# Kernel optimization log

Hardware: AMD Instinct MI355X
Metric: run time of the kernel (lower is better)

## Reference

```python
import jax, jax.numpy as jnp
import numpy as np

HEADS = 4
DIM_HEAD = 64
SCALE = DIM_HEAD ** -0.5


def setup_inputs() -> dict:
    key = jax.random.key(0)
    k1, k2, k3 = jax.random.split(key, 3)
    C = 256
    hidden = HEADS * DIM_HEAD  # 256
    x = jax.random.normal(k1, (16, C, 64, 64), dtype=jnp.float32)
    # 1x1 conv weights collapsed to [out, in] matrices
    w_qkv = jax.random.normal(k2, (3 * hidden, C), dtype=jnp.float32) * (C ** -0.5)
    w_out = jax.random.normal(k3, (C, hidden), dtype=jnp.float32) * (hidden ** -0.5)
    b_out = jnp.zeros((C,), dtype=jnp.float32)
    return {"x": x, "w_qkv": w_qkv, "w_out": w_out, "b_out": b_out}


def reference(x, w_qkv, w_out, b_out):
    b, c, h, w = x.shape
    n = h * w
    # 1x1 conv == channel GEMM
    qkv = jnp.einsum('bchw,oc->bohw', x, w_qkv)           # [b, 3*hidden, h, w]
    qkv = qkv.reshape(b, 3, HEADS, DIM_HEAD, n)            # [b, 3, H, d, n]
    q, k, v = qkv[:, 0], qkv[:, 1], qkv[:, 2]              # each [b, H, d, n]
    q = jax.nn.softmax(q, axis=2) * SCALE                  # softmax over d
    k = jax.nn.softmax(k, axis=3)                          # softmax over n
    context = jnp.einsum('bhdn,bhen->bhde', k, v)          # [b, H, d, e]
    out = jnp.einsum('bhde,bhdn->bhen', context, q)        # [b, H, e, n]
    out = out.reshape(b, HEADS * DIM_HEAD, h, w)           # [b, hidden, h, w]
    return jnp.einsum('bchw,oc->bohw', out, w_out) + b_out[None, :, None, None]
```

## Files before the change

### kernel.cpp

```cpp
#include <hip/hip_runtime.h>

#define NPIX 4096
#define SCALE 0.125f

typedef _Float16 half8 __attribute__((ext_vector_type(8)));
typedef _Float16 half4 __attribute__((ext_vector_type(4)));
typedef float floatx4 __attribute__((ext_vector_type(4)));

__device__ __forceinline__ void async16(void* lds, const void* g) {
  __builtin_amdgcn_global_load_lds(
      (const __attribute__((address_space(1))) unsigned int*)(uintptr_t)g,
      (__attribute__((address_space(3))) unsigned int*)(unsigned)(uintptr_t)lds,
      16, 0, 0);
}

__global__ __launch_bounds__(256) void split16_kernel(const float* __restrict__ w,
                                                      _Float16* __restrict__ hi,
                                                      _Float16* __restrict__ lo, int n) {
  int i = blockIdx.x * 256 + threadIdx.x;
  if (i < n) {
    float v = w[i];
    _Float16 h = (_Float16)v;
    hi[i] = h;
    lo[i] = (_Float16)(v - (float)h);
  }
}

__global__ __launch_bounds__(256) void transpose16_kernel(const float* __restrict__ x,
                                                          _Float16* __restrict__ xt) {
  __shared__ float t[64][65];
  const int n0 = blockIdx.x * 64, c0 = blockIdx.y * 64, b = blockIdx.z;
  const float* xp = x + (long)b * 256 * NPIX;
  const int tid = threadIdx.x;
  const int r = tid >> 4, c4 = (tid & 15) * 4;
#pragma unroll
  for (int p = 0; p < 4; p++) {
    float4 v = *(const float4*)&xp[(long)(c0 + r + p * 16) * NPIX + n0 + c4];
    t[r + p * 16][c4 + 0] = v.x;
    t[r + p * 16][c4 + 1] = v.y;
    t[r + p * 16][c4 + 2] = v.z;
    t[r + p * 16][c4 + 3] = v.w;
  }
  __syncthreads();
  const int n = tid >> 2, cg = (tid & 3) * 16;
  alignas(16) _Float16 o[16];
#pragma unroll
  for (int i = 0; i < 16; i++) o[i] = (_Float16)t[cg + i][n];
  _Float16* dst = &xt[((long)b * NPIX + n0 + n) * 256 + c0 + cg];
  *(float4*)dst = *(float4*)&o[0];
  *(float4*)(dst + 8) = *(float4*)&o[8];
}

__global__ __launch_bounds__(256) void q_gemm_softmax(const _Float16* __restrict__ Ahp,
                                                      const _Float16* __restrict__ Alp,
                                                      const _Float16* __restrict__ Bt,
                                                      _Float16* __restrict__ PT) {
  union alignas(16) QU {
    struct {
      _Float16 Ah[128 * 32];
      _Float16 Al[128 * 32];
      _Float16 Bt[128 * 32];
    } st;
    _Float16 pt[128][128];
  };
  __shared__ QU u;
  const int tid = threadIdx.x;
  const int n0 = blockIdx.x * 128, m0 = blockIdx.y * 128;
  const int bz = blockIdx.z;
  const _Float16* Bp = Bt + (long)bz * NPIX * 256;
  const int wv = tid >> 6, l = tid & 63;
  const int r16 = l & 15, q = l >> 4;
  const int mb = (wv >> 1) * 64, nb = (wv & 1) * 64;
  const int r1 = tid >> 2;
  const int o1 = ((tid & 3) * 8) ^ (((r1 >> 1) & 3) * 8);
  const int r2 = r1 + 64;
  const int ldsc1 = (wv * 64) * 8;
  const int ldsc2 = (256 + wv * 64) * 8;
  const int q8 = (q * 8) ^ (((r16 >> 1) & 3) * 8);

  floatx4 acc[4][4];
#pragma unroll
  for (int i = 0; i < 4; i++)
#pragma unroll
    for (int j = 0; j < 4; j++) acc[i][j] = (floatx4){0.f, 0.f, 0.f, 0.f};

  for (int kt = 0; kt < 8; kt++) {
    const int k0 = kt * 32;
    async16(&u.st.Ah[ldsc1], &Ahp[(long)(m0 + r1) * 256 + k0 + o1]);
    async16(&u.st.Ah[ldsc2], &Ahp[(long)(m0 + r2) * 256 + k0 + o1]);
    async16(&u.st.Al[ldsc1], &Alp[(long)(m0 + r1) * 256 + k0 + o1]);
    async16(&u.st.Al[ldsc2], &Alp[(long)(m0 + r2) * 256 + k0 + o1]);
    async16(&u.st.Bt[ldsc1], &Bp[(long)(n0 + r1) * 256 + k0 + o1]);
    async16(&u.st.Bt[ldsc2], &Bp[(long)(n0 + r2) * 256 + k0 + o1]);
    __syncthreads();
    half8 fa[4], flo[4], fb[4];
#pragma unroll
    for (int i = 0; i < 4; i++) {
      fa[i] = *(const half8*)&u.st.Ah[(mb + i * 16 + r16) * 32 + q8];
      flo[i] = *(const half8*)&u.st.Al[(mb + i * 16 + r16) * 32 + q8];
      fb[i] = *(const half8*)&u.st.Bt[(nb + i * 16 + r16) * 32 + q8];
    }
#pragma unroll
    for (int i = 0; i < 4; i++)
#pragma unroll
      for (int j = 0; j < 4; j++) {
        acc[i][j] = __builtin_amdgcn_mfma_f32_16x16x32_f16(fa[i], fb[j], acc[i][j], 0, 0, 0);
        acc[i][j] = __builtin_amdgcn_mfma_f32_16x16x32_f16(flo[i], fb[j], acc[i][j], 0, 0, 0);
      }
    __syncthreads();
  }

#pragma unroll
  for (int j = 0; j < 4; j++) {
    float s = 0.f;
#pragma unroll
    for (int i = 0; i < 4; i++)
#pragma unroll
      for (int t = 0; t < 4; t++) {
        float e = __expf(acc[i][j][t]);
        acc[i][j][t] = e;
        s += e;
      }
    s += __shfl_xor(s, 16, 64);
    s += __shfl_xor(s, 32, 64);
    const float rinv = 1.0f / s;
    const int nl = nb + j * 16 + r16;
    const int swz = (nl & 7) * 8;
#pragma unroll
    for (int i = 0; i < 4; i++) {
      half4 h4;
#pragma unroll
      for (int t = 0; t < 4; t++) h4[t] = (_Float16)(acc[i][j][t] * rinv);
      *(half4*)&u.pt[nl][(mb + i * 16 + q * 4) ^ swz] = h4;
    }
  }
  __syncthreads();
  const int rbase = tid >> 4, c16 = tid & 15;
  _Float16* dst = PT + ((long)(bz * 2 + (m0 >> 7)) * NPIX + n0) * 128;
#pragma unroll
  for (int k = 0; k < 8; k++) {
    const int row = rbase + k * 16;
    const int chunk = c16 ^ (row & 7);
    float4 v = *(const float4*)&u.pt[row][chunk * 8];
    *(float4*)&dst[(long)row * 128 + c16 * 8] = v;
  }
}

__global__ __launch_bounds__(256) void kv_ctx_gemm(const _Float16* __restrict__ Ahp,
                                                   const _Float16* __restrict__ Alp,
                                                   const _Float16* __restrict__ Bt,
                                                   float* __restrict__ pbuf,
                                                   float* __restrict__ rsbuf) {
  union alignas(16) KVU {
    struct {
      _Float16 Ah[128 * 32];
      _Float16 Al[128 * 32];
      _Float16 Bt[128 * 32];
    } st;
    _Float16 ev[128][136];
  };
  __shared__ KVU u;
  const int tid = threadIdx.x;
  const int chunk = blockIdx.x;
  const int hi = blockIdx.y;
  const int b = blockIdx.z;
  const int n0 = chunk * 128;
  const _Float16* Bp = Bt + (long)b * NPIX * 256;
  const int wv = tid >> 6, l = tid & 63;
  const int r16 = l & 15, q = l >> 4;
  const int mb = (wv >> 1) * 64, nb = (wv & 1) * 64;
  const int r1 = tid >> 2;
  const int o1 = ((tid & 3) * 8) ^ (((r1 >> 1) & 3) * 8);
  const int ldsc1 = (wv * 64) * 8;
  const int ldsc2 = (256 + wv * 64) * 8;
  const int q8 = (q * 8) ^ (((r16 >> 1) & 3) * 8);
  const long gAk = (long)(256 + hi * 64 + r1) * 256;
  const long gAv = (long)(512 + hi * 64 + r1) * 256;

  floatx4 acc[4][4];
#pragma unroll
  for (int i = 0; i < 4; i++)
#pragma unroll
    for (int j = 0; j < 4; j++) acc[i][j] = (floatx4){0.f, 0.f, 0.f, 0.f};

  for (int kt = 0; kt < 8; kt++) {
    const int k0 = kt * 32;
    async16(&u.st.Ah[ldsc1], &Ahp[gAk + k0 + o1]);
    async16(&u.st.Ah[ldsc2], &Ahp[gAv + k0 + o1]);
    async16(&u.st.Al[ldsc1], &Alp[gAk + k0 + o1]);
    async16(&u.st.Al[ldsc2], &Alp[gAv + k0 + o1]);
    async16(&u.st.Bt[ldsc1], &Bp[(long)(n0 + r1) * 256 + k0 + o1]);
    async16(&u.st.Bt[ldsc2], &Bp[(long)(n0 + 64 + r1) * 256 + k0 + o1]);
    __syncthreads();
    half8 fa[4], flo[4], fb[4];
#pragma unroll
    for (int i = 0; i < 4; i++) {
      fa[i] = *(const half8*)&u.st.Ah[(mb + i * 16 + r16) * 32 + q8];
      flo[i] = *(const half8*)&u.st.Al[(mb + i * 16 + r16) * 32 + q8];
      fb[i] = *(const half8*)&u.st.Bt[(nb + i * 16 + r16) * 32 + q8];
    }
#pragma unroll
    for (int i = 0; i < 4; i++)
#pragma unroll
      for (int j = 0; j < 4; j++) {
        acc[i][j] = __builtin_amdgcn_mfma_f32_16x16x32_f16(fa[i], fb[j], acc[i][j], 0, 0, 0);
        acc[i][j] = __builtin_amdgcn_mfma_f32_16x16x32_f16(flo[i], fb[j], acc[i][j], 0, 0, 0);
      }
    __syncthreads();
  }

  const bool is_k = (mb == 0);
#pragma unroll
  for (int i = 0; i < 4; i++) {
    const int row = mb + i * 16 + q * 4;
#pragma unroll
    for (int j = 0; j < 4; j++) {
      const int col = nb + j * 16 + r16;
#pragma unroll
      for (int t = 0; t < 4; t++) {
        const float vv0 = acc[i][j][t];
        u.ev[row + t][col] = (_Float16)(is_k ? __expf(vv0) : vv0);
      }
    }
  }
  __syncthreads();

  floatx4 c2[4];
#pragma unroll
  for (int j = 0; j < 4; j++) c2[j] = (floatx4){0.f, 0.f, 0.f, 0.f};
  float rs = 0.f;
#pragma unroll
  for (int ks = 0; ks < 4; ks++) {
    half8 a = *(const half8*)&u.ev[wv * 16 + r16][ks * 32 + q * 8];
#pragma unroll
    for (int ii = 0; ii < 8; ii++) rs += (float)a[ii];
#pragma unroll
    for (int j = 0; j < 4; j++) {
      half8 bv = *(const half8*)&u.ev[64 + j * 16 + r16][ks * 32 + q * 8];
      c2[j] = __builtin_amdgcn_mfma_f32_16x16x32_f16(a, bv, c2[j], 0, 0, 0);
    }
  }
  rs += __shfl_xor(rs, 16, 64);
  rs += __shfl_xor(rs, 32, 64);
  const int bh = b * 4 + hi;
  float* pp = pbuf + ((long)bh * 32 + chunk) * 4096;
#pragma unroll
  for (int j = 0; j < 4; j++)
#pragma unroll
    for (int reg = 0; reg < 4; reg++)
      pp[(wv * 16 + q * 4 + reg) * 64 + j * 16 + r16] = c2[j][reg];
  if (l < 16) rsbuf[((long)bh * 32 + chunk) * 64 + wv * 16 + r16] = rs;
}

__global__ __launch_bounds__(256) void reduce_ctx(const float* __restrict__ pbuf,
                                                  float* __restrict__ ctx) {
  int g = blockIdx.x * 256 + threadIdx.x;
  int bh = g >> 12, e = g & 4095;
  const float* pp = pbuf + ((long)bh * 32) * 4096 + e;
  float s = 0.f;
#pragma unroll
  for (int c = 0; c < 32; c++) s += pp[(long)c * 4096];
  ctx[g] = s;
}

__global__ __launch_bounds__(256) void zinv_kernel(const float* __restrict__ rsbuf,
                                                   float* __restrict__ kinvz) {
  int g = blockIdx.x * 256 + threadIdx.x;
  int bh = g >> 6, d = g & 63;
  const float* rp = rsbuf + (long)bh * 32 * 64 + d;
  float s = 0.f;
#pragma unroll
  for (int c = 0; c < 32; c++) s += rp[c * 64];
  kinvz[g] = 1.0f / s;
}

__global__ __launch_bounds__(256) void mctx_kernel(const float* __restrict__ w_out,
                                                   const float* __restrict__ ctx,
                                                   const float* __restrict__ kinvz,
                                                   _Float16* __restrict__ Mhi,
                                                   _Float16* __restrict__ Mlo) {
  __shared__ float sctxT[64][65];
  const int cq = blockIdx.x, h = blockIdx.y, b = blockIdx.z;
  const int bh = b * 4 + h;
  const float* cp = ctx + (long)bh * 4096;
  const int tid = threadIdx.x;
  {
    const int d = tid >> 2, e0 = (tid & 3) * 16;
#pragma unroll
    for (int k = 0; k < 4; k++) {
      float4 v = *(const float4*)&cp[d * 64 + e0 + k * 4];
      sctxT[e0 + k * 4 + 0][d] = v.x;
      sctxT[e0 + k * 4 + 1][d] = v.y;
      sctxT[e0 + k * 4 + 2][d] = v.z;
      sctxT[e0 + k * 4 + 3][d] = v.w;
    }
  }
  __syncthreads();
  const int c = cq * 64 + (tid >> 2);
  const int d0 = (tid & 3) * 16;
  const float* wp = w_out + (long)c * 256 + h * 64;
  float acc[16];
#pragma unroll
  for (int i = 0; i < 16; i++) acc[i] = 0.f;
#pragma unroll
  for (int e4 = 0; e4 < 16; e4++) {
    float4 wv = *(const float4*)&wp[e4 * 4];
#pragma unroll
    for (int u2 = 0; u2 < 4; u2++) {
      const float we = ((const float*)&wv)[u2];
      const int e = e4 * 4 + u2;
#pragma unroll
      for (int dd = 0; dd < 16; dd++) acc[dd] = fmaf(we, sctxT[e][d0 + dd], acc[dd]);
    }
  }
  alignas(16) _Float16 hi16[16], lo16[16];
#pragma unroll
  for (int k4 = 0; k4 < 4; k4++) {
    float4 zv = *(const float4*)&kinvz[bh * 64 + d0 + k4 * 4];
#pragma unroll
    for (int u2 = 0; u2 < 4; u2++) {
      const int dd = k4 * 4 + u2;
      float v = acc[dd] * (SCALE * ((const float*)&zv)[u2]);
      _Float16 hh = (_Float16)v;
      hi16[dd] = hh;
      lo16[dd] = (_Float16)(v - (float)hh);
    }
  }
  _Float16* mh = Mhi + ((long)b * 256 + c) * 256 + h * 64 + d0;
  _Float16* ml = Mlo + ((long)b * 256 + c) * 256 + h * 64 + d0;
#pragma unroll
  for (int k = 0; k < 2; k++) {
    *(float4*)&mh[k * 8] = *(float4*)&hi16[k * 8];
    *(float4*)&ml[k * 8] = *(float4*)&lo16[k * 8];
  }
}

__global__ __launch_bounds__(256) void out_gemm(const _Float16* __restrict__ Mhi,
                                                const _Float16* __restrict__ Mlo,
                                                const _Float16* __restrict__ PT,
                                                float* __restrict__ C,
                                                const float* __restrict__ bias) {
  __shared__ _Float16 sAh[128 * 32];
  __shared__ _Float16 sAl[128 * 32];
  __shared__ _Float16 sBt[128 * 32];
  const int tid = threadIdx.x;
  const int n0 = blockIdx.x * 128, m0 = blockIdx.y * 128;
  const int b = blockIdx.z;
  const _Float16* Ah = Mhi + (long)b * 65536;
  const _Float16* Al = Mlo + (long)b * 65536;
  float* Cp = C + (long)b * 256 * NPIX;
  const int wv = tid >> 6, l = tid & 63;
  const int r16 = l & 15, q = l >> 4;
  const int mb = (wv >> 1) * 64, nb = (wv & 1) * 64;
  const int r1 = tid >> 2;
  const int o1 = ((tid & 3) * 8) ^ (((r1 >> 1) & 3) * 8);
  const int r2 = r1 + 64;
  const int ldsc1 = (wv * 64) * 8;
  const int ldsc2 = (256 + wv * 64) * 8;
  const int q8 = (q * 8) ^ (((r16 >> 1) & 3) * 8);

  floatx4 acc[4][4];
#pragma unroll
  for (int i = 0; i < 4; i++)
#pragma unroll
    for (int j = 0; j < 4; j++) acc[i][j] = (floatx4){0.f, 0.f, 0.f, 0.f};

  for (int kt = 0; kt < 8; kt++) {
    const int k0 = kt * 32;
    async16(&sAh[ldsc1], &Ah[(long)(m0 + r1) * 256 + k0 + o1]);
    async16(&sAh[ldsc2], &Ah[(long)(m0 + r2) * 256 + k0 + o1]);
    async16(&sAl[ldsc1], &Al[(long)(m0 + r1) * 256 + k0 + o1]);
    async16(&sAl[ldsc2], &Al[(long)(m0 + r2) * 256 + k0 + o1]);
    const _Float16* Bk = PT + ((long)(b * 2 + (kt >> 2)) * NPIX + n0) * 128;
    async16(&sBt[ldsc1], &Bk[(long)r1 * 128 + (kt & 3) * 32 + o1]);
    async16(&sBt[ldsc2], &Bk[(long)(r1 + 64) * 128 + (kt & 3) * 32 + o1]);
    __syncthreads();
    half8 fa[4], flo[4], fb[4];
#pragma unroll
    for (int i = 0; i < 4; i++) {
      fa[i] = *(const half8*)&sAh[(mb + i * 16 + r16) * 32 + q8];
      flo[i] = *(const half8*)&sAl[(mb + i * 16 + r16) * 32 + q8];
      fb[i] = *(const half8*)&sBt[(nb + i * 16 + r16) * 32 + q8];
    }
#pragma unroll
    for (int i = 0; i < 4; i++)
#pragma unroll
      for (int j = 0; j < 4; j++) {
        acc[i][j] = __builtin_amdgcn_mfma_f32_16x16x32_f16(fa[i], fb[j], acc[i][j], 0, 0, 0);
        acc[i][j] = __builtin_amdgcn_mfma_f32_16x16x32_f16(flo[i], fb[j], acc[i][j], 0, 0, 0);
      }
    __syncthreads();
  }
#pragma unroll
  for (int i = 0; i < 4; i++) {
    const int mrow = m0 + mb + i * 16 + q * 4;
#pragma unroll
    for (int t = 0; t < 4; t++) {
      float bz = bias[mrow + t];
#pragma unroll
      for (int j = 0; j < 4; j++) {
        Cp[(long)(mrow + t) * NPIX + n0 + nb + j * 16 + r16] = acc[i][j][t] + bz;
      }
    }
  }
}

extern "C" void kernel_launch(void* const* d_in, const int* in_sizes, int n_in,
                              void* d_out, int out_size, void* d_ws, size_t ws_size,
                              hipStream_t stream) {
  const float* x = (const float*)d_in[0];
  const float* w_qkv = (const float*)d_in[1];
  const float* w_out = (const float*)d_in[2];
  const float* b_out = (const float*)d_in[3];
  float* out = (float*)d_out;

  _Float16* PT = (_Float16*)d_ws;
  float* ctx = (float*)(PT + (long)16 * 2 * NPIX * 128);
  float* kinvz = ctx + 64 * 4096;
  float* rsbuf = kinvz + 4096;
  _Float16* wq_hi = (_Float16*)(rsbuf + 64 * 32 * 64);
  _Float16* wq_lo = wq_hi + 768 * 256;
  _Float16* Mhi = wq_lo + 768 * 256;
  _Float16* Mlo = Mhi + 16 * 256 * 256;
  _Float16* xt = (_Float16*)d_out;
  float* pbuf = (float*)d_out + (1 << 23);

  split16_kernel<<<768, 256, 0, stream>>>(w_qkv, wq_hi, wq_lo, 768 * 256);
  transpose16_kernel<<<dim3(64, 4, 16), 256, 0, stream>>>(x, xt);
  kv_ctx_gemm<<<dim3(32, 4, 16), 256, 0, stream>>>(wq_hi, wq_lo, xt, pbuf, rsbuf);
  reduce_ctx<<<1024, 256, 0, stream>>>(pbuf, ctx);
  zinv_kernel<<<16, 256, 0, stream>>>(rsbuf, kinvz);
  q_gemm_softmax<<<dim3(32, 2, 16), 256, 0, stream>>>(wq_hi, wq_lo, xt, PT);
  mctx_kernel<<<dim3(4, 4, 16), 256, 0, stream>>>(w_out, ctx, kinvz, Mhi, Mlo);
  out_gemm<<<dim3(32, 2, 16), 256, 0, stream>>>(Mhi, Mlo, PT, out, b_out);
}
```

Measured before the change: 232.1 us.

## Double-buffer LDS staging in GEMMs and process four chunks per kv_ctx block

Adds double-buffered async global-to-LDS staging to the q_gemm_softmax, kv_ctx_gemm and out_gemm kernels, so the next k-tile is fetched while the current one feeds the MFMAs. This also removes one barrier per k-step. kv_ctx_gemm now loops over four pixel chunks per block and keeps the context accumulator in registers, which cuts the partial-sum buffer and the reduce/zinv work by a factor of four. The costs are doubled LDS use, which can lower occupancy, and a smaller kv_ctx grid of 512 blocks.

```diff
diff --git a/kernel.cpp b/kernel.cpp
--- a/kernel.cpp
+++ b/kernel.cpp
@@ -56,11 +56,7 @@
                                                       const _Float16* __restrict__ Bt,
                                                       _Float16* __restrict__ PT) {
   union alignas(16) QU {
-    struct {
-      _Float16 Ah[128 * 32];
-      _Float16 Al[128 * 32];
-      _Float16 Bt[128 * 32];
-    } st;
+    _Float16 st[2][3][128 * 32];
     _Float16 pt[128][128];
   };
   __shared__ QU u;
@@ -78,27 +74,33 @@
   const int ldsc2 = (256 + wv * 64) * 8;
   const int q8 = (q * 8) ^ (((r16 >> 1) & 3) * 8);
 
+  auto STAGE = [&](int buf, int kt) {
+    const int k0 = kt * 32;
+    async16(&u.st[buf][0][ldsc1], &Ahp[(long)(m0 + r1) * 256 + k0 + o1]);
+    async16(&u.st[buf][0][ldsc2], &Ahp[(long)(m0 + r2) * 256 + k0 + o1]);
+    async16(&u.st[buf][1][ldsc1], &Alp[(long)(m0 + r1) * 256 + k0 + o1]);
+    async16(&u.st[buf][1][ldsc2], &Alp[(long)(m0 + r2) * 256 + k0 + o1]);
+    async16(&u.st[buf][2][ldsc1], &Bp[(long)(n0 + r1) * 256 + k0 + o1]);
+    async16(&u.st[buf][2][ldsc2], &Bp[(long)(n0 + r2) * 256 + k0 + o1]);
+  };
+
   floatx4 acc[4][4];
 #pragma unroll
   for (int i = 0; i < 4; i++)
 #pragma unroll
     for (int j = 0; j < 4; j++) acc[i][j] = (floatx4){0.f, 0.f, 0.f, 0.f};
 
+  STAGE(0, 0);
+  __syncthreads();
+  int cur = 0;
   for (int kt = 0; kt < 8; kt++) {
-    const int k0 = kt * 32;
-    async16(&u.st.Ah[ldsc1], &Ahp[(long)(m0 + r1) * 256 + k0 + o1]);
-    async16(&u.st.Ah[ldsc2], &Ahp[(long)(m0 + r2) * 256 + k0 + o1]);
-    async16(&u.st.Al[ldsc1], &Alp[(long)(m0 + r1) * 256 + k0 + o1]);
-    async16(&u.st.Al[ldsc2], &Alp[(long)(m0 + r2) * 256 + k0 + o1]);
-    async16(&u.st.Bt[ldsc1], &Bp[(long)(n0 + r1) * 256 + k0 + o1]);
-    async16(&u.st.Bt[ldsc2], &Bp[(long)(n0 + r2) * 256 + k0 + o1]);
-    __syncthreads();
+    if (kt < 7) STAGE(cur ^ 1, kt + 1);
     half8 fa[4], flo[4], fb[4];
 #pragma unroll
     for (int i = 0; i < 4; i++) {
-      fa[i] = *(const half8*)&u.st.Ah[(mb + i * 16 + r16) * 32 + q8];
-      flo[i] = *(const half8*)&u.st.Al[(mb + i * 16 + r16) * 32 + q8];
-      fb[i] = *(const half8*)&u.st.Bt[(nb + i * 16 + r16) * 32 + q8];
+      fa[i] = *(const half8*)&u.st[cur][0][(mb + i * 16 + r16) * 32 + q8];
+      flo[i] = *(const half8*)&u.st[cur][1][(mb + i * 16 + r16) * 32 + q8];
+      fb[i] = *(const half8*)&u.st[cur][2][(nb + i * 16 + r16) * 32 + q8];
     }
 #pragma unroll
     for (int i = 0; i < 4; i++)
@@ -108,6 +110,7 @@
         acc[i][j] = __builtin_amdgcn_mfma_f32_16x16x32_f16(flo[i], fb[j], acc[i][j], 0, 0, 0);
       }
     __syncthreads();
+    cur ^= 1;
   }
 
 #pragma unroll
@@ -146,25 +149,21 @@
   }
 }
 
+#define CPB 4
 __global__ __launch_bounds__(256) void kv_ctx_gemm(const _Float16* __restrict__ Ahp,
                                                    const _Float16* __restrict__ Alp,
                                                    const _Float16* __restrict__ Bt,
                                                    float* __restrict__ pbuf,
                                                    float* __restrict__ rsbuf) {
   union alignas(16) KVU {
-    struct {
-      _Float16 Ah[128 * 32];
-      _Float16 Al[128 * 32];
-      _Float16 Bt[128 * 32];
-    } st;
+    _Float16 st[2][3][128 * 32];
     _Float16 ev[128][136];
   };
   __shared__ KVU u;
   const int tid = threadIdx.x;
-  const int chunk = blockIdx.x;
+  const int cg = blockIdx.x;
   const int hi = blockIdx.y;
   const int b = blockIdx.z;
-  const int n0 = chunk * 128;
   const _Float16* Bp = Bt + (long)b * NPIX * 256;
   const int wv = tid >> 6, l = tid & 63;
   const int r16 = l & 15, q = l >> 4;
@@ -177,89 +176,102 @@
   const long gAk = (long)(256 + hi * 64 + r1) * 256;
   const long gAv = (long)(512 + hi * 64 + r1) * 256;
 
-  floatx4 acc[4][4];
-#pragma unroll
-  for (int i = 0; i < 4; i++)
-#pragma unroll
-    for (int j = 0; j < 4; j++) acc[i][j] = (floatx4){0.f, 0.f, 0.f, 0.f};
-
-  for (int kt = 0; kt < 8; kt++) {
+  auto STAGE = [&](int buf, int kt, int n0) {
     const int k0 = kt * 32;
-    async16(&u.st.Ah[ldsc1], &Ahp[gAk + k0 + o1]);
-    async16(&u.st.Ah[ldsc2], &Ahp[gAv + k0 + o1]);
-    async16(&u.st.Al[ldsc1], &Alp[gAk + k0 + o1]);
-    async16(&u.st.Al[ldsc2], &Alp[gAv + k0 + o1]);
-    async16(&u.st.Bt[ldsc1], &Bp[(long)(n0 + r1) * 256 + k0 + o1]);
-    async16(&u.st.Bt[ldsc2], &Bp[(long)(n0 + 64 + r1) * 256 + k0 + o1]);
-    __syncthreads();
-    half8 fa[4], flo[4], fb[4];
-#pragma unroll
-    for (int i = 0; i < 4; i++) {
-      fa[i] = *(const half8*)&u.st.Ah[(mb + i * 16 + r16) * 32 + q8];
-      flo[i] = *(const half8*)&u.st.Al[(mb + i * 16 + r16) * 32 + q8];
-      fb[i] = *(const half8*)&u.st.Bt[(nb + i * 16 + r16) * 32 + q8];
-    }
-#pragma unroll
-    for (int i = 0; i < 4; i++)
-#pragma unroll
-      for (int j = 0; j < 4; j++) {
-        acc[i][j] = __builtin_amdgcn_mfma_f32_16x16x32_f16(fa[i], fb[j], acc[i][j], 0, 0, 0);
-        acc[i][j] = __builtin_amdgcn_mfma_f32_16x16x32_f16(flo[i], fb[j], acc[i][j], 0, 0, 0);
-      }
-    __syncthreads();
-  }
-
-  const bool is_k = (mb == 0);
-#pragma unroll
-  for (int i = 0; i < 4; i++) {
-    const int row = mb + i * 16 + q * 4;
-#pragma unroll
-    for (int j = 0; j < 4; j++) {
-      const int col = nb + j * 16 + r16;
-#pragma unroll
-      for (int t = 0; t < 4; t++) {
-        const float vv0 = acc[i][j][t];
-        u.ev[row + t][col] = (_Float16)(is_k ? __expf(vv0) : vv0);
-      }
-    }
-  }
-  __syncthreads();
+    async16(&u.st[buf][0][ldsc1], &Ahp[gAk + k0 + o1]);
+    async16(&u.st[buf][0][ldsc2], &Ahp[gAv + k0 + o1]);
+    async16(&u.st[buf][1][ldsc1], &Alp[gAk + k0 + o1]);
+    async16(&u.st[buf][1][ldsc2], &Alp[gAv + k0 + o1]);
+    async16(&u.st[buf][2][ldsc1], &Bp[(long)(n0 + r1) * 256 + k0 + o1]);
+    async16(&u.st[buf][2][ldsc2], &Bp[(long)(n0 + 64 + r1) * 256 + k0 + o1]);
+  };
 
   floatx4 c2[4];
 #pragma unroll
   for (int j = 0; j < 4; j++) c2[j] = (floatx4){0.f, 0.f, 0.f, 0.f};
   float rs = 0.f;
-#pragma unroll
-  for (int ks = 0; ks < 4; ks++) {
-    half8 a = *(const half8*)&u.ev[wv * 16 + r16][ks * 32 + q * 8];
-#pragma unroll
-    for (int ii = 0; ii < 8; ii++) rs += (float)a[ii];
-#pragma unroll
-    for (int j = 0; j < 4; j++) {
-      half8 bv = *(const half8*)&u.ev[64 + j * 16 + r16][ks * 32 + q * 8];
-      c2[j] = __builtin_amdgcn_mfma_f32_16x16x32_f16(a, bv, c2[j], 0, 0, 0);
-    }
-  }
+
+  for (int cs = 0; cs < CPB; cs++) {
+    const int n0 = (cg * CPB + cs) * 128;
+    floatx4 acc[4][4];
+#pragma unroll
+    for (int i = 0; i < 4; i++)
+#pragma unroll
+      for (int j = 0; j < 4; j++) acc[i][j] = (floatx4){0.f, 0.f, 0.f, 0.f};
+
+    STAGE(0, 0, n0);
+    __syncthreads();
+    int cur = 0;
+    for (int kt = 0; kt < 8; kt++) {
+      if (kt < 7) STAGE(cur ^ 1, kt + 1, n0);
+      half8 fa[4], flo[4], fb[4];
+#pragma unroll
+      for (int i = 0; i < 4; i++) {
+        fa[i] = *(const half8*)&u.st[cur][0][(mb + i * 16 + r16) * 32 + q8];
+        flo[i] = *(const half8*)&u.st[cur][1][(mb + i * 16 + r16) * 32 + q8];
+        fb[i] = *(const half8*)&u.st[cur][2][(nb + i * 16 + r16) * 32 + q8];
+      }
+#pragma unroll
+      for (int i = 0; i < 4; i++)
+#pragma unroll
+        for (int j = 0; j < 4; j++) {
+          acc[i][j] = __builtin_amdgcn_mfma_f32_16x16x32_f16(fa[i], fb[j], acc[i][j], 0, 0, 0);
+          acc[i][j] = __builtin_amdgcn_mfma_f32_16x16x32_f16(flo[i], fb[j], acc[i][j], 0, 0, 0);
+        }
+      __syncthreads();
+      cur ^= 1;
+    }
+
+    const bool is_k = (mb == 0);
+#pragma unroll
+    for (int i = 0; i < 4; i++) {
+      const int row = mb + i * 16 + q * 4;
+#pragma unroll
+      for (int j = 0; j < 4; j++) {
+        const int col = nb + j * 16 + r16;
+#pragma unroll
+        for (int t = 0; t < 4; t++) {
+          const float vv0 = acc[i][j][t];
+          u.ev[row + t][col] = (_Float16)(is_k ? __expf(vv0) : vv0);
+        }
+      }
+    }
+    __syncthreads();
+
+#pragma unroll
+    for (int ks = 0; ks < 4; ks++) {
+      half8 a = *(const half8*)&u.ev[wv * 16 + r16][ks * 32 + q * 8];
+#pragma unroll
+      for (int ii = 0; ii < 8; ii++) rs += (float)a[ii];
+#pragma unroll
+      for (int j = 0; j < 4; j++) {
+        half8 bv = *(const half8*)&u.ev[64 + j * 16 + r16][ks * 32 + q * 8];
+        c2[j] = __builtin_amdgcn_mfma_f32_16x16x32_f16(a, bv, c2[j], 0, 0, 0);
+      }
+    }
+    __syncthreads();
+  }
+
   rs += __shfl_xor(rs, 16, 64);
   rs += __shfl_xor(rs, 32, 64);
   const int bh = b * 4 + hi;
-  float* pp = pbuf + ((long)bh * 32 + chunk) * 4096;
+  float* pp = pbuf + ((long)bh * 8 + cg) * 4096;
 #pragma unroll
   for (int j = 0; j < 4; j++)
 #pragma unroll
     for (int reg = 0; reg < 4; reg++)
       pp[(wv * 16 + q * 4 + reg) * 64 + j * 16 + r16] = c2[j][reg];
-  if (l < 16) rsbuf[((long)bh * 32 + chunk) * 64 + wv * 16 + r16] = rs;
+  if (l < 16) rsbuf[((long)bh * 8 + cg) * 64 + wv * 16 + r16] = rs;
 }
 
 __global__ __launch_bounds__(256) void reduce_ctx(const float* __restrict__ pbuf,
                                                   float* __restrict__ ctx) {
   int g = blockIdx.x * 256 + threadIdx.x;
   int bh = g >> 12, e = g & 4095;
-  const float* pp = pbuf + ((long)bh * 32) * 4096 + e;
+  const float* pp = pbuf + ((long)bh * 8) * 4096 + e;
   float s = 0.f;
 #pragma unroll
-  for (int c = 0; c < 32; c++) s += pp[(long)c * 4096];
+  for (int c = 0; c < 8; c++) s += pp[(long)c * 4096];
   ctx[g] = s;
 }
 
@@ -267,10 +279,10 @@
                                                    float* __restrict__ kinvz) {
   int g = blockIdx.x * 256 + threadIdx.x;
   int bh = g >> 6, d = g & 63;
-  const float* rp = rsbuf + (long)bh * 32 * 64 + d;
+  const float* rp = rsbuf + (long)bh * 8 * 64 + d;
   float s = 0.f;
 #pragma unroll
-  for (int c = 0; c < 32; c++) s += rp[c * 64];
+  for (int c = 0; c < 8; c++) s += rp[c * 64];
   kinvz[g] = 1.0f / s;
 }
 
@@ -340,9 +352,7 @@
                                                 const _Float16* __restrict__ PT,
                                                 float* __restrict__ C,
                                                 const float* __restrict__ bias) {
-  __shared__ _Float16 sAh[128 * 32];
-  __shared__ _Float16 sAl[128 * 32];
-  __shared__ _Float16 sBt[128 * 32];
+  __shared__ _Float16 st[2][3][128 * 32];
   const int tid = threadIdx.x;
   const int n0 = blockIdx.x * 128, m0 = blockIdx.y * 128;
   const int b = blockIdx.z;
@@ -359,28 +369,34 @@
   const int ldsc2 = (256 + wv * 64) * 8;
   const int q8 = (q * 8) ^ (((r16 >> 1) & 3) * 8);
 
+  auto STAGE = [&](int buf, int kt) {
+    const int k0 = kt * 32;
+    async16(&st[buf][0][ldsc1], &Ah[(long)(m0 + r1) * 256 + k0 + o1]);
+    async16(&st[buf][0][ldsc2], &Ah[(long)(m0 + r2) * 256 + k0 + o1]);
+    async16(&st[buf][1][ldsc1], &Al[(long)(m0 + r1) * 256 + k0 + o1]);
+    async16(&st[buf][1][ldsc2], &Al[(long)(m0 + r2) * 256 + k0 + o1]);
+    const _Float16* Bk = PT + ((long)(b * 2 + (kt >> 2)) * NPIX + n0) * 128;
+    async16(&st[buf][2][ldsc1], &Bk[(long)r1 * 128 + (kt & 3) * 32 + o1]);
+    async16(&st[buf][2][ldsc2], &Bk[(long)(r1 + 64) * 128 + (kt & 3) * 32 + o1]);
+  };
+
   floatx4 acc[4][4];
 #pragma unroll
   for (int i = 0; i < 4; i++)
 #pragma unroll
     for (int j = 0; j < 4; j++) acc[i][j] = (floatx4){0.f, 0.f, 0.f, 0.f};
 
+  STAGE(0, 0);
+  __syncthreads();
+  int cur = 0;
   for (int kt = 0; kt < 8; kt++) {
-    const int k0 = kt * 32;
-    async16(&sAh[ldsc1], &Ah[(long)(m0 + r1) * 256 + k0 + o1]);
-    async16(&sAh[ldsc2], &Ah[(long)(m0 + r2) * 256 + k0 + o1]);
-    async16(&sAl[ldsc1], &Al[(long)(m0 + r1) * 256 + k0 + o1]);
-    async16(&sAl[ldsc2], &Al[(long)(m0 + r2) * 256 + k0 + o1]);
-    const _Float16* Bk = PT + ((long)(b * 2 + (kt >> 2)) * NPIX + n0) * 128;
-    async16(&sBt[ldsc1], &Bk[(long)r1 * 128 + (kt & 3) * 32 + o1]);
-    async16(&sBt[ldsc2], &Bk[(long)(r1 + 64) * 128 + (kt & 3) * 32 + o1]);
-    __syncthreads();
+    if (kt < 7) STAGE(cur ^ 1, kt + 1);
     half8 fa[4], flo[4], fb[4];
 #pragma unroll
     for (int i = 0; i < 4; i++) {
-      fa[i] = *(const half8*)&sAh[(mb + i * 16 + r16) * 32 + q8];
-      flo[i] = *(const half8*)&sAl[(mb + i * 16 + r16) * 32 + q8];
-      fb[i] = *(const half8*)&sBt[(nb + i * 16 + r16) * 32 + q8];
+      fa[i] = *(const half8*)&st[cur][0][(mb + i * 16 + r16) * 32 + q8];
+      flo[i] = *(const half8*)&st[cur][1][(mb + i * 16 + r16) * 32 + q8];
+      fb[i] = *(const half8*)&st[cur][2][(nb + i * 16 + r16) * 32 + q8];
     }
 #pragma unroll
     for (int i = 0; i < 4; i++)
@@ -390,6 +406,7 @@
         acc[i][j] = __builtin_amdgcn_mfma_f32_16x16x32_f16(flo[i], fb[j], acc[i][j], 0, 0, 0);
       }
     __syncthreads();
+    cur ^= 1;
   }
 #pragma unroll
   for (int i = 0; i < 4; i++) {
@@ -418,7 +435,7 @@
   float* ctx = (float*)(PT + (long)16 * 2 * NPIX * 128);
   float* kinvz = ctx + 64 * 4096;
   float* rsbuf = kinvz + 4096;
-  _Float16* wq_hi = (_Float16*)(rsbuf + 64 * 32 * 64);
+  _Float16* wq_hi = (_Float16*)(rsbuf + 64 * 8 * 64);
   _Float16* wq_lo = wq_hi + 768 * 256;
   _Float16* Mhi = wq_lo + 768 * 256;
   _Float16* Mlo = Mhi + 16 * 256 * 256;
@@ -427,7 +444,7 @@
 
   split16_kernel<<<768, 256, 0, stream>>>(w_qkv, wq_hi, wq_lo, 768 * 256);
   transpose16_kernel<<<dim3(64, 4, 16), 256, 0, stream>>>(x, xt);
-  kv_ctx_gemm<<<dim3(32, 4, 16), 256, 0, stream>>>(wq_hi, wq_lo, xt, pbuf, rsbuf);
+  kv_ctx_gemm<<<dim3(8, 4, 16), 256, 0, stream>>>(wq_hi, wq_lo, xt, pbuf, rsbuf);
   reduce_ctx<<<1024, 256, 0, stream>>>(pbuf, ctx);
   zinv_kernel<<<16, 256, 0, stream>>>(rsbuf, kinvz);
   q_gemm_softmax<<<dim3(32, 2, 16), 256, 0, stream>>>(wq_hi, wq_lo, xt, PT);
```

Result: faster. 214.6 us (-7.5%).
